# Kernel tuning notes

Measured on AMD Instinct MI355X. Metric: run time of the kernel, lower is better.

Reference implementation:

```python
import jax, jax.numpy as jnp
import numpy as np

N, D, E = 100000, 128, 800000

def setup_inputs() -> dict:
    key = jax.random.key(0)
    k1, k2, k3, k4 = jax.random.split(key, 4)
    z = jax.random.normal(k1, (N, D), dtype=jnp.float32)
    edge_index = jax.random.randint(k2, (2, E), 0, N, dtype=jnp.int64)
    # PyTorch-style init scale for Linear layers (kaiming-uniform-ish via normal is fine for a numeric reference)
    W1 = jax.random.normal(k3, (2 * D, D), dtype=jnp.float32) * (1.0 / np.sqrt(2 * D))
    b1 = jnp.zeros((D,), dtype=jnp.float32)
    W2 = jax.random.normal(k4, (D, 1), dtype=jnp.float32) * (1.0 / np.sqrt(D))
    b2 = jnp.zeros((1,), dtype=jnp.float32)
    return {"z": z, "edge_index": edge_index, "W1": W1, "b1": b1, "W2": W2, "b2": b2}

def reference(z, edge_index, W1, b1, W2, b2):
    # row/col gather of node embeddings
    row, col = edge_index[0], edge_index[1]
    # cat([z[row], z[col]]) @ W1 == z[row] @ W1[:D] + z[col] @ W1[D:]
    # -> avoids materializing the [E, 2D] concatenated tensor
    d = z.shape[1]
    h = z[row] @ W1[:d] + z[col] @ W1[d:] + b1          # [E, D]
    h = jax.nn.relu(h)                                   # Dropout(0.1) is identity in eval mode
    out = h @ W2 + b2                                    # [E, 1]
    return out.squeeze(-1)                               # [E]
```

## Files before the change

kernel.cpp:

```cpp
#include <hip/hip_runtime.h>

#define DDIM 128

typedef __bf16 bf16x8 __attribute__((ext_vector_type(8)));
typedef float  floatx4 __attribute__((ext_vector_type(4)));

__device__ inline unsigned short f2bf(float f) {
    unsigned u = __builtin_bit_cast(unsigned, f);
    u += 0x7fffu + ((u >> 16) & 1u);
    return (unsigned short)(u >> 16);
}

__global__ __launch_bounds__(256) void swizzle_w(
    const float* __restrict__ W1, unsigned short* __restrict__ Wf)
{
    const int id   = blockIdx.x * 256 + threadIdx.x;
    const int f    = id >> 6;
    const int lane = id & 63;
    const int nt = f >> 2, ks = f & 3;
    const int n  = nt * 16 + (lane & 15);
    const int kb = ks * 32 + ((lane >> 4) & 3) * 8;
    const float* __restrict__ wsrc = (n < DDIM)
        ? (W1 + (size_t)kb * DDIM + n)
        : (W1 + (size_t)(DDIM + kb) * DDIM + (n - DDIM));
    unsigned short frag[8];
    #pragma unroll
    for (int j = 0; j < 8; ++j)
        frag[j] = f2bf(wsrc[(size_t)j * DDIM]);
    *(uint4*)&Wf[(size_t)id * 8] = *(const uint4*)frag;
}

__global__ __launch_bounds__(256, 3) void precompute_uv_mfma_q8(
    const float* __restrict__ z, const unsigned short* __restrict__ Wf,
    const float* __restrict__ b1,
    signed char* __restrict__ U8, signed char* __restrict__ V8,
    float* __restrict__ u_scale, float* __restrict__ v_scale,
    int N, int nchunks)
{
    const int lane = threadIdx.x & 63;
    const int w    = threadIdx.x >> 6;
    const int mrow = lane & 15;
    const int quad = lane >> 4;

    float bu[8];
    #pragma unroll
    for (int nt = 0; nt < 8; ++nt) bu[nt] = b1[nt * 16 + mrow];

    int chunk = blockIdx.x;
    if (chunk >= nchunks) return;

    const int koff = quad * 8;

    float4 raw[8];
    {
        int grow = chunk * 64 + w * 16 + mrow; if (grow > N - 1) grow = N - 1;
        const float* zrow = z + (size_t)grow * DDIM;
        #pragma unroll
        for (int ks = 0; ks < 4; ++ks) {
            raw[ks * 2]     = *(const float4*)(zrow + ks * 32 + koff);
            raw[ks * 2 + 1] = *(const float4*)(zrow + ks * 32 + koff + 4);
        }
    }

    while (true) {
        const int next = chunk + gridDim.x;
        const bool have_next = next < nchunks;

        bf16x8 afrag[4];
        #pragma unroll
        for (int ks = 0; ks < 4; ++ks) {
            const float4 x0 = raw[ks * 2], x1 = raw[ks * 2 + 1];
            unsigned short a[8];
            a[0] = f2bf(x0.x); a[1] = f2bf(x0.y); a[2] = f2bf(x0.z); a[3] = f2bf(x0.w);
            a[4] = f2bf(x1.x); a[5] = f2bf(x1.y); a[6] = f2bf(x1.z); a[7] = f2bf(x1.w);
            afrag[ks] = __builtin_bit_cast(bf16x8, *(const uint4*)a);
        }

        float4 raw2[8];
        if (have_next) {
            int grow = next * 64 + w * 16 + mrow; if (grow > N - 1) grow = N - 1;
            const float* zrow = z + (size_t)grow * DDIM;
            #pragma unroll
            for (int ks = 0; ks < 4; ++ks) {
                raw2[ks * 2]     = *(const float4*)(zrow + ks * 32 + koff);
                raw2[ks * 2 + 1] = *(const float4*)(zrow + ks * 32 + koff + 4);
            }
        }

        const int m0 = chunk * 64 + w * 16;

        #pragma unroll 1
        for (int half = 0; half < 2; ++half) {
            signed char* __restrict__ dst8 = half ? V8 : U8;
            float*       __restrict__ dscl = half ? v_scale : u_scale;

            floatx4 acc[8];
            #pragma unroll
            for (int nt = 0; nt < 8; ++nt) acc[nt] = (floatx4){0.f, 0.f, 0.f, 0.f};

            const unsigned short* __restrict__ wbase =
                Wf + ((size_t)half * 32 * 64) * 8 + (size_t)lane * 8;

            #pragma unroll
            for (int ks = 0; ks < 4; ++ks) {
                #pragma unroll
                for (int nt = 0; nt < 8; ++nt) {
                    const bf16x8 b = __builtin_bit_cast(bf16x8,
                        *(const uint4*)(wbase + (size_t)((nt * 4 + ks) * 64) * 8));
                    acc[nt] = __builtin_amdgcn_mfma_f32_16x16x32_bf16(afrag[ks], b, acc[nt], 0, 0, 0);
                }
            }

            #pragma unroll
            for (int r = 0; r < 4; ++r) {
                float v[8];
                #pragma unroll
                for (int nt = 0; nt < 8; ++nt)
                    v[nt] = half ? acc[nt][r] : (acc[nt][r] + bu[nt]);

                float mx = 0.f;
                #pragma unroll
                for (int nt = 0; nt < 8; ++nt) mx = fmaxf(mx, fabsf(v[nt]));
                #pragma unroll
                for (int m = 1; m < 16; m <<= 1)
                    mx = fmaxf(mx, __shfl_xor(mx, m, 16));
                mx = fmaxf(mx, 1e-20f);
                const float inv = 127.f / mx;

                unsigned char bytes[8];
                #pragma unroll
                for (int nt = 0; nt < 8; ++nt)
                    bytes[nt] = (unsigned char)(((int)rintf(v[nt] * inv)) & 0xff);

                const int grow = m0 + quad * 4 + r;
                if (grow < N) {
                    *(unsigned long long*)&dst8[(size_t)grow * DDIM + mrow * 8] =
                        *(const unsigned long long*)bytes;
                    if (mrow == 0) dscl[grow] = mx * (1.f / 127.f);
                }
            }
        }

        if (!have_next) break;
        #pragma unroll
        for (int i = 0; i < 8; ++i) raw[i] = raw2[i];
        chunk = next;
    }
}

__global__ __launch_bounds__(256) void edge_kernel_i8(
    const int* __restrict__ ei,
    const signed char* __restrict__ U8, const signed char* __restrict__ V8,
    const float* __restrict__ u_scale, const float* __restrict__ v_scale,
    const float* __restrict__ W2, const float* __restrict__ b2,
    float* __restrict__ out, int E)
{
    const int t  = threadIdx.x;
    const int p  = t & 15;
    const int g0 = (blockIdx.x * 16 + (t >> 4)) * 4;

    float ww[8];
    #pragma unroll
    for (int j = 0; j < 8; ++j) ww[j] = W2[j * 16 + p];

    if (g0 >= E) return;

    int rows[4], cols[4];
    if (g0 + 3 < E) {
        const int4 r4 = *(const int4*)(ei + g0);
        const int4 c4 = *(const int4*)(ei + (size_t)E + g0);
        rows[0]=r4.x; rows[1]=r4.y; rows[2]=r4.z; rows[3]=r4.w;
        cols[0]=c4.x; cols[1]=c4.y; cols[2]=c4.z; cols[3]=c4.w;
    } else {
        #pragma unroll
        for (int i = 0; i < 4; ++i) {
            const int gi = (g0 + i < E) ? (g0 + i) : (E - 1);
            rows[i] = ei[gi];
            cols[i] = ei[(size_t)E + gi];
        }
    }

    uint2 uu[4], vv[4];
    #pragma unroll
    for (int i = 0; i < 4; ++i)
        uu[i] = *(const uint2*)(U8 + (size_t)rows[i] * DDIM + p * 8);
    #pragma unroll
    for (int i = 0; i < 4; ++i)
        vv[i] = *(const uint2*)(V8 + (size_t)cols[i] * DDIM + p * 8);

    float su[4], sv[4];
    #pragma unroll
    for (int i = 0; i < 4; ++i) { su[i] = u_scale[rows[i]]; sv[i] = v_scale[cols[i]]; }

    const float bias = b2[0];

    #pragma unroll
    for (int i = 0; i < 4; ++i) {
        const signed char* us = (const signed char*)&uu[i];
        const signed char* vs = (const signed char*)&vv[i];
        float s = 0.f;
        #pragma unroll
        for (int j = 0; j < 8; ++j) {
            const float h = fmaf(sv[i], (float)vs[j], su[i] * (float)us[j]);
            s = fmaf(fmaxf(h, 0.f), ww[j], s);
        }
        #pragma unroll
        for (int off = 8; off > 0; off >>= 1)
            s += __shfl_down(s, off, 16);
        if (p == 0 && g0 + i < E) out[g0 + i] = s + bias;
    }
}

__global__ __launch_bounds__(256) void edge_fused_fallback(
    const float* __restrict__ z, const int* __restrict__ ei,
    const float* __restrict__ W1, const float* __restrict__ b1,
    const float* __restrict__ W2, const float* __restrict__ b2,
    float* __restrict__ out, int N, int E)
{
    const int tid  = blockIdx.x * 256 + threadIdx.x;
    const int e    = tid >> 6;
    const int lane = tid & 63;
    if (e >= E) return;

    const int row = ei[e];
    const int col = ei[(size_t)E + e];
    const float* zr = z + (size_t)row * DDIM;
    const float* zc = z + (size_t)col * DDIM;

    float h0 = b1[lane];
    float h1 = b1[lane + 64];
    for (int k = 0; k < DDIM; ++k) {
        const float a = zr[k];
        const float b = zc[k];
        h0 = fmaf(a, W1[k * DDIM + lane],               h0);
        h0 = fmaf(b, W1[(DDIM + k) * DDIM + lane],      h0);
        h1 = fmaf(a, W1[k * DDIM + lane + 64],          h1);
        h1 = fmaf(b, W1[(DDIM + k) * DDIM + lane + 64], h1);
    }
    float s = fmaxf(h0, 0.f) * W2[lane] + fmaxf(h1, 0.f) * W2[lane + 64];
    #pragma unroll
    for (int off = 32; off > 0; off >>= 1)
        s += __shfl_down(s, off, 64);
    if (lane == 0) out[e] = s + b2[0];
}

extern "C" void kernel_launch(void* const* d_in, const int* in_sizes, int n_in,
                              void* d_out, int out_size, void* d_ws, size_t ws_size,
                              hipStream_t stream)
{
    const float* z  = (const float*)d_in[0];
    const int*   ei = (const int*)d_in[1];
    const float* W1 = (const float*)d_in[2];
    const float* b1 = (const float*)d_in[3];
    const float* W2 = (const float*)d_in[4];
    const float* b2 = (const float*)d_in[5];
    float*       out = (float*)d_out;

    const int N = in_sizes[0] / DDIM;
    const int E = in_sizes[1] / 2;

    const size_t n128 = (size_t)N * DDIM;
    const size_t need = 2 * n128 + 2 * (size_t)N * sizeof(float)
                      + 64 * 1024 + 512;
    if (ws_size >= need) {
        signed char* U8 = (signed char*)d_ws;
        signed char* V8 = U8 + n128;
        float* usc = (float*)(((size_t)(V8 + n128) + 255) & ~(size_t)255);
        float* vsc = usc + N;
        unsigned short* Wf = (unsigned short*)(((size_t)(vsc + N) + 255) & ~(size_t)255);

        const int nchunks = (N + 63) / 64;
        hipLaunchKernelGGL(swizzle_w, dim3(16), dim3(256), 0, stream, W1, Wf);
        hipLaunchKernelGGL(precompute_uv_mfma_q8, dim3(512), dim3(256), 0, stream,
                           z, Wf, b1, U8, V8, usc, vsc, N, nchunks);
        hipLaunchKernelGGL(edge_kernel_i8, dim3((E + 63) / 64), dim3(256), 0, stream,
                           ei, U8, V8, usc, vsc, W2, b2, out, E);
    } else {
        hipLaunchKernelGGL(edge_fused_fallback, dim3((E + 3) / 4), dim3(256), 0, stream,
                           z, ei, W1, b1, W2, b2, out, N, E);
    }
}
```

Before: 148.5 us.

## Fuse weight swizzle into precompute kernel and split U/V halves across blocks

Removes the separate swizzle_w launch: each block converts its half of W1 to bf16 MFMA fragments in shared memory at startup. The grid becomes 2 x 384 so each block computes only U or only V, and B fragments now come from LDS instead of global memory. This saves one kernel launch and the global fragment reads, but each z row is now loaded and converted twice (once per half), and every block repeats the weight conversion.

```diff
diff --git a/kernel.cpp b/kernel.cpp
--- a/kernel.cpp
+++ b/kernel.cpp
@@ -11,44 +11,51 @@
     return (unsigned short)(u >> 16);
 }
 
-__global__ __launch_bounds__(256) void swizzle_w(
-    const float* __restrict__ W1, unsigned short* __restrict__ Wf)
-{
-    const int id   = blockIdx.x * 256 + threadIdx.x;
-    const int f    = id >> 6;
-    const int lane = id & 63;
-    const int nt = f >> 2, ks = f & 3;
-    const int n  = nt * 16 + (lane & 15);
-    const int kb = ks * 32 + ((lane >> 4) & 3) * 8;
-    const float* __restrict__ wsrc = (n < DDIM)
-        ? (W1 + (size_t)kb * DDIM + n)
-        : (W1 + (size_t)(DDIM + kb) * DDIM + (n - DDIM));
-    unsigned short frag[8];
-    #pragma unroll
-    for (int j = 0; j < 8; ++j)
-        frag[j] = f2bf(wsrc[(size_t)j * DDIM]);
-    *(uint4*)&Wf[(size_t)id * 8] = *(const uint4*)frag;
-}
-
 __global__ __launch_bounds__(256, 3) void precompute_uv_mfma_q8(
-    const float* __restrict__ z, const unsigned short* __restrict__ Wf,
+    const float* __restrict__ z, const float* __restrict__ W1,
     const float* __restrict__ b1,
     signed char* __restrict__ U8, signed char* __restrict__ V8,
     float* __restrict__ u_scale, float* __restrict__ v_scale,
     int N, int nchunks)
 {
-    const int lane = threadIdx.x & 63;
-    const int w    = threadIdx.x >> 6;
+    __shared__ unsigned short WsF[32 * 64 * 8];
+
+    const int t    = threadIdx.x;
+    const int lane = t & 63;
+    const int w    = t >> 6;
     const int mrow = lane & 15;
     const int quad = lane >> 4;
+    const int half = blockIdx.x;
+    signed char* __restrict__ dst8 = half ? V8 : U8;
+    float*       __restrict__ dscl = half ? v_scale : u_scale;
+    const float* __restrict__ Wh   = W1 + (size_t)half * DDIM * DDIM;
+
+    {
+        const int nlow = mrow;
+        const int kq   = quad;
+        #pragma unroll
+        for (int i = 0; i < 8; ++i) {
+            const int ntks = w + i * 4;
+            const int nt = ntks >> 2, ks = ntks & 3;
+            const int n  = nt * 16 + nlow;
+            const int kb = ks * 32 + kq * 8;
+            unsigned short frag[8];
+            #pragma unroll
+            for (int j = 0; j < 8; ++j)
+                frag[j] = f2bf(Wh[(size_t)(kb + j) * DDIM + n]);
+            *(uint4*)&WsF[(ntks * 64 + lane) * 8] = *(const uint4*)frag;
+        }
+    }
 
     float bu[8];
     #pragma unroll
-    for (int nt = 0; nt < 8; ++nt) bu[nt] = b1[nt * 16 + mrow];
-
-    int chunk = blockIdx.x;
+    for (int nt = 0; nt < 8; ++nt)
+        bu[nt] = half ? 0.f : b1[nt * 16 + mrow];
+
+    __syncthreads();
+
+    int chunk = blockIdx.y;
     if (chunk >= nchunks) return;
-
     const int koff = quad * 8;
 
     float4 raw[8];
@@ -63,7 +70,7 @@
     }
 
     while (true) {
-        const int next = chunk + gridDim.x;
+        const int next = chunk + gridDim.y;
         const bool have_next = next < nchunks;
 
         bf16x8 afrag[4];
@@ -87,57 +94,46 @@
             }
         }
 
+        floatx4 acc[8];
+        #pragma unroll
+        for (int nt = 0; nt < 8; ++nt) acc[nt] = (floatx4){0.f, 0.f, 0.f, 0.f};
+
+        #pragma unroll
+        for (int ks = 0; ks < 4; ++ks) {
+            #pragma unroll
+            for (int nt = 0; nt < 8; ++nt) {
+                const bf16x8 b = __builtin_bit_cast(bf16x8,
+                    *(const uint4*)&WsF[((nt * 4 + ks) * 64 + lane) * 8]);
+                acc[nt] = __builtin_amdgcn_mfma_f32_16x16x32_bf16(afrag[ks], b, acc[nt], 0, 0, 0);
+            }
+        }
+
         const int m0 = chunk * 64 + w * 16;
-
-        #pragma unroll 1
-        for (int half = 0; half < 2; ++half) {
-            signed char* __restrict__ dst8 = half ? V8 : U8;
-            float*       __restrict__ dscl = half ? v_scale : u_scale;
-
-            floatx4 acc[8];
-            #pragma unroll
-            for (int nt = 0; nt < 8; ++nt) acc[nt] = (floatx4){0.f, 0.f, 0.f, 0.f};
-
-            const unsigned short* __restrict__ wbase =
-                Wf + ((size_t)half * 32 * 64) * 8 + (size_t)lane * 8;
-
-            #pragma unroll
-            for (int ks = 0; ks < 4; ++ks) {
-                #pragma unroll
-                for (int nt = 0; nt < 8; ++nt) {
-                    const bf16x8 b = __builtin_bit_cast(bf16x8,
-                        *(const uint4*)(wbase + (size_t)((nt * 4 + ks) * 64) * 8));
-                    acc[nt] = __builtin_amdgcn_mfma_f32_16x16x32_bf16(afrag[ks], b, acc[nt], 0, 0, 0);
-                }
-            }
-
-            #pragma unroll
-            for (int r = 0; r < 4; ++r) {
-                float v[8];
-                #pragma unroll
-                for (int nt = 0; nt < 8; ++nt)
-                    v[nt] = half ? acc[nt][r] : (acc[nt][r] + bu[nt]);
-
-                float mx = 0.f;
-                #pragma unroll
-                for (int nt = 0; nt < 8; ++nt) mx = fmaxf(mx, fabsf(v[nt]));
-                #pragma unroll
-                for (int m = 1; m < 16; m <<= 1)
-                    mx = fmaxf(mx, __shfl_xor(mx, m, 16));
-                mx = fmaxf(mx, 1e-20f);
-                const float inv = 127.f / mx;
-
-                unsigned char bytes[8];
-                #pragma unroll
-                for (int nt = 0; nt < 8; ++nt)
-                    bytes[nt] = (unsigned char)(((int)rintf(v[nt] * inv)) & 0xff);
-
-                const int grow = m0 + quad * 4 + r;
-                if (grow < N) {
-                    *(unsigned long long*)&dst8[(size_t)grow * DDIM + mrow * 8] =
-                        *(const unsigned long long*)bytes;
-                    if (mrow == 0) dscl[grow] = mx * (1.f / 127.f);
-                }
+        #pragma unroll
+        for (int r = 0; r < 4; ++r) {
+            float v[8];
+            #pragma unroll
+            for (int nt = 0; nt < 8; ++nt) v[nt] = acc[nt][r] + bu[nt];
+
+            float mx = 0.f;
+            #pragma unroll
+            for (int nt = 0; nt < 8; ++nt) mx = fmaxf(mx, fabsf(v[nt]));
+            #pragma unroll
+            for (int m = 1; m < 16; m <<= 1)
+                mx = fmaxf(mx, __shfl_xor(mx, m, 16));
+            mx = fmaxf(mx, 1e-20f);
+            const float inv = 127.f / mx;
+
+            unsigned char bytes[8];
+            #pragma unroll
+            for (int nt = 0; nt < 8; ++nt)
+                bytes[nt] = (unsigned char)(((int)rintf(v[nt] * inv)) & 0xff);
+
+            const int grow = m0 + quad * 4 + r;
+            if (grow < N) {
+                *(unsigned long long*)&dst8[(size_t)grow * DDIM + mrow * 8] =
+                    *(const unsigned long long*)bytes;
+                if (mrow == 0) dscl[grow] = mx * (1.f / 127.f);
             }
         }
 
@@ -260,19 +256,16 @@
     const int E = in_sizes[1] / 2;
 
     const size_t n128 = (size_t)N * DDIM;
-    const size_t need = 2 * n128 + 2 * (size_t)N * sizeof(float)
-                      + 64 * 1024 + 512;
+    const size_t need = 2 * n128 + 2 * (size_t)N * sizeof(float) + 256;
     if (ws_size >= need) {
         signed char* U8 = (signed char*)d_ws;
         signed char* V8 = U8 + n128;
         float* usc = (float*)(((size_t)(V8 + n128) + 255) & ~(size_t)255);
         float* vsc = usc + N;
-        unsigned short* Wf = (unsigned short*)(((size_t)(vsc + N) + 255) & ~(size_t)255);
 
         const int nchunks = (N + 63) / 64;
-        hipLaunchKernelGGL(swizzle_w, dim3(16), dim3(256), 0, stream, W1, Wf);
-        hipLaunchKernelGGL(precompute_uv_mfma_q8, dim3(512), dim3(256), 0, stream,
-                           z, Wf, b1, U8, V8, usc, vsc, N, nchunks);
+        hipLaunchKernelGGL(precompute_uv_mfma_q8, dim3(2, 384), dim3(256), 0, stream,
+                           z, W1, b1, U8, V8, usc, vsc, N, nchunks);
         hipLaunchKernelGGL(edge_kernel_i8, dim3((E + 63) / 64), dim3(256), 0, stream,
                            ei, U8, V8, usc, vsc, W2, b2, out, E);
     } else {
```

New measurement: 185.3 us. 24.8% more time.
